# Kernel optimization log

Measured on AMD Instinct MI355X. Metric: run time of the kernel, lower is better.

## Reference

```python
import jax, jax.numpy as jnp
import numpy as np

B, T, DM = 4, 2048, 1024
H, DK, DV = 16, 64, 64


def setup_inputs() -> dict:
    key = jax.random.key(0)
    k1, k2, k3, k4 = jax.random.split(key, 4)
    x = jax.random.normal(k1, (B, T, DM), dtype=jnp.float32)
    scale = 0.02
    Wq = jax.random.normal(k2, (H, DM, DK), dtype=jnp.float32) * scale
    Wk = jax.random.normal(k3, (H, DM, DK), dtype=jnp.float32) * scale
    Wv = jax.random.normal(k4, (H, DM, DV), dtype=jnp.float32) * scale
    return {"x": x, "Wq": Wq, "Wk": Wk, "Wv": Wv}


def reference(x, Wq, Wk, Wv):
    # Per-head projections, vectorized over heads: [B,H,T,dk]
    q = jnp.einsum('btd,hdk->bhtk', x, Wq)
    k = jnp.einsum('btd,hdk->bhtk', x, Wk)
    v = jnp.einsum('btd,hdv->bhtv', x, Wv)
    scale = DK ** -0.5  # k.shape[-1] ** -0.5 in original
    wei = jnp.einsum('bhtk,bhsk->bhts', q, k) * scale  # [B,H,T,T]
    causal = jnp.tril(jnp.ones((T, T), dtype=bool))
    wei = jnp.where(causal, wei, -jnp.inf)
    wei = jax.nn.softmax(wei, axis=-1)
    # dropout p=0.0 -> identity (eval-mode equivalent)
    out = jnp.einsum('bhts,bhsv->bhtv', wei, v)  # [B,H,T,dv]
    # concat heads along last dim: [B,T,H*dv]
    return out.transpose(0, 2, 1, 3).reshape(B, T, H * DV)
```

## Files before the change

### kernel.cpp

```cpp
#include <hip/hip_runtime.h>


#define B_  4
#define T_  2048
#define DM_ 1024
#define H_  16
#define D_  64
#define DMO 1024

typedef unsigned short u16;
typedef unsigned int   u32;
typedef u16   u16x8  __attribute__((ext_vector_type(8)));
typedef short s16x8  __attribute__((ext_vector_type(8)));
typedef float f32x4  __attribute__((ext_vector_type(4)));
typedef float f32x16 __attribute__((ext_vector_type(16)));
typedef u32   u32x2  __attribute__((ext_vector_type(2)));
typedef u32   u32x4  __attribute__((ext_vector_type(4)));

#if __has_builtin(__builtin_amdgcn_exp2f)
#define EXP2(x) __builtin_amdgcn_exp2f(x)
#else
#define EXP2(x) __expf((x) * 0.69314718f)
#endif

#define WAIT_BAR(N) do {                                                      \
    asm volatile("s_waitcnt vmcnt(" #N ")" ::: "memory");                     \
    __builtin_amdgcn_s_barrier();                                             \
    __builtin_amdgcn_sched_barrier(0); } while (0)
#define BAR_ONLY() do {                                                       \
    __builtin_amdgcn_s_barrier();                                             \
    __builtin_amdgcn_sched_barrier(0); } while (0)

__device__ __forceinline__ u16 f2bf_hu(float f) {
    u32 u = __builtin_bit_cast(u32, f) + 0x8000u;
    return (u16)(u >> 16);
}
__device__ __forceinline__ u32 pk2(float lo, float hi) {
    u32 ul = __builtin_bit_cast(u32, lo) + 0x8000u;
    u32 uh = __builtin_bit_cast(u32, hi) + 0x8000u;
    return __builtin_amdgcn_perm(uh, ul, 0x07060302);
}
__device__ __forceinline__ u16x8 cvt8(const float* s) {
    f32x4 a = *(const f32x4*)s;
    f32x4 b = *(const f32x4*)(s + 4);
    u32x4 r { pk2(a[0], a[1]), pk2(a[2], a[3]), pk2(b[0], b[1]), pk2(b[2], b[3]) };
    return __builtin_bit_cast(u16x8, r);
}
__device__ __forceinline__ f32x4 mfma16(u16x8 a, u16x8 b, f32x4 c) {
    return __builtin_amdgcn_mfma_f32_16x16x32_bf16(
        __builtin_bit_cast(s16x8, a), __builtin_bit_cast(s16x8, b), c, 0, 0, 0);
}
__device__ __forceinline__ f32x16 mfma32(u16x8 a, u16x8 b, f32x16 c) {
    return __builtin_amdgcn_mfma_f32_32x32x16_bf16(
        __builtin_bit_cast(s16x8, a), __builtin_bit_cast(s16x8, b), c, 0, 0, 0);
}
__device__ __forceinline__ void gld_lds16(const u16* g, u16* l) {
    __builtin_amdgcn_global_load_lds(
        (const __attribute__((address_space(1))) u32*)g,
        (__attribute__((address_space(3))) u32*)l, 16, 0, 0);
}

__global__ __launch_bounds__(256) void cvt_all(
    const float* __restrict__ x,  const float* __restrict__ Wq,
    const float* __restrict__ Wk, const float* __restrict__ Wv,
    u16* __restrict__ xb, u16* __restrict__ Wt)
{
    __shared__ u16 L[64][74];
    const int bx = blockIdx.x;
    if (bx < 1024) {
        size_t i0 = ((size_t)bx * 256 + threadIdx.x) * 32;
        #pragma unroll
        for (int c = 0; c < 4; c++)
            *(u16x8*)(xb + i0 + c * 8) = cvt8(x + i0 + c * 8);
        return;
    }
    const int wb = bx - 1024;
    const int dblk = wb & 15, h = (wb >> 4) & 15, mat = wb >> 8;
    const float* W = (mat == 0) ? Wq : (mat == 1) ? Wk : Wv;
    const int tid = threadIdx.x;
    {
        const int dl = tid >> 2, c = (tid & 3) * 16;
        const float* src = W + ((size_t)h * DM_ + dblk * 64 + dl) * D_ + c;
        #pragma unroll
        for (int g = 0; g < 2; g++)
            *(u16x8*)&L[dl][c + g * 8] = cvt8(src + g * 8);
    }
    __syncthreads();
    {
        const int dkr = tid >> 2, g = tid & 3;
        u16 tmp[16];
        #pragma unroll
        for (int j = 0; j < 16; j++) tmp[j] = L[g * 16 + j][dkr];
        u16* dst = Wt + ((size_t)(mat * 16 + h) * 64 + dkr) * DM_ + dblk * 64 + g * 16;
        *(u16x8*)dst = *(u16x8*)tmp;
        *(u16x8*)(dst + 8) = *(u16x8*)(tmp + 8);
    }
}

template<int SWAP>
__device__ __forceinline__ void pcompute(const char* Asb, const char* Bsb,
                                         int wm, int wn, int quad, int l16,
                                         int ax, f32x4 (&acc)[4][4]) {
    #pragma unroll
    for (int ks = 0; ks < 2; ks++) {
        u16x8 af[4], bf[4];
        #pragma unroll
        for (int i = 0; i < 4; i++)
            af[i] = *(const u16x8*)(Asb +
                ((((wm * 64 + i * 16 + l16) * 64 + ks * 32 + quad * 8) * 2) ^ ax));
        #pragma unroll
        for (int j = 0; j < 4; j++)
            bf[j] = *(const u16x8*)(Bsb +
                ((((wn * 64 + j * 16 + l16) * 64 + ks * 32 + quad * 8) * 2) ^ ax));
        __builtin_amdgcn_s_setprio(1);
        #pragma unroll
        for (int i = 0; i < 4; i++)
            #pragma unroll
            for (int j = 0; j < 4; j++)
                acc[i][j] = SWAP ? mfma16(bf[j], af[i], acc[i][j])
                                 : mfma16(af[i], bf[j], acc[i][j]);
        __builtin_amdgcn_s_setprio(0);
    }
}

__global__ __launch_bounds__(256) void proj_kernel(
    const u16* __restrict__ xb, const u16* __restrict__ Wt,
    u16* __restrict__ Qc, u16* __restrict__ Kc, u16* __restrict__ Vtc)
{
    __shared__ __attribute__((aligned(16))) u16 As0[128][64];
    __shared__ __attribute__((aligned(16))) u16 Bs0[128][64];
    __shared__ __attribute__((aligned(16))) u16 As1[128][64];
    __shared__ __attribute__((aligned(16))) u16 Bs1[128][64];

    const int pb = blockIdx.x;
    const int wg = (pb & 7) * 192 + (pb >> 3);
    const int m0 = (wg & 63) * 128;
    const int n0 = (wg >> 6) * 128;
    const int mat = n0 >> 10;
    const int tid  = threadIdx.x;
    const int wave = tid >> 6, lane = tid & 63;
    const int quad = lane >> 4, l16 = lane & 15;
    const int wm   = wave >> 1, wn = wave & 1;

    const int r8 = lane >> 3, g8 = lane & 7;
    const int gs = (g8 ^ r8) * 8;
    const int ax = (l16 & 7) << 4;

    f32x4 acc[4][4];
    #pragma unroll
    for (int i = 0; i < 4; i++)
        #pragma unroll
        for (int j = 0; j < 4; j++) acc[i][j] = f32x4{0.f, 0.f, 0.f, 0.f};

    auto STAGE = [&](u16* Ad, u16* Bd, int kb) {
        const int kbase = kb * 64;
        #pragma unroll
        for (int it = 0; it < 4; it++) {
            const int row = it * 32 + wave * 8 + r8;
            const int ldo = (it * 4 + wave) * 512 + lane * 8;
            gld_lds16(xb + (size_t)(m0 + row) * DM_ + kbase + gs, Ad + ldo);
            gld_lds16(Wt + (size_t)(n0 + row) * DM_ + kbase + gs, Bd + ldo);
        }
    };

    STAGE(&As0[0][0], &Bs0[0][0], 0);
    STAGE(&As1[0][0], &Bs1[0][0], 1);

    #define PLOOP(SW)                                                        \
        for (int j = 0; j < 8; j++) {                                        \
            WAIT_BAR(8);                                                     \
            pcompute<SW>((const char*)As0, (const char*)Bs0,                 \
                         wm, wn, quad, l16, ax, acc);                        \
            BAR_ONLY();                                                      \
            if (2 * j + 2 < 16) STAGE(&As0[0][0], &Bs0[0][0], 2 * j + 2);    \
            if (j < 7) { WAIT_BAR(8); } else { WAIT_BAR(0); }                \
            pcompute<SW>((const char*)As1, (const char*)Bs1,                 \
                         wm, wn, quad, l16, ax, acc);                        \
            BAR_ONLY();                                                      \
            if (2 * j + 3 < 16) STAGE(&As1[0][0], &Bs1[0][0], 2 * j + 3);    \
        }
    if (mat != 2) { PLOOP(1) } else { PLOOP(0) }
    #undef PLOOP

    const int h_base = (n0 & 1023) >> 6;
    if (mat != 2) {
        u16* Cm = (mat == 0) ? Qc : Kc;
        const float sc = (mat == 0) ? 0.18033688f : 1.0f;
        #pragma unroll
        for (int i = 0; i < 4; i++) {
            const int m  = m0 + wm * 64 + i * 16 + l16;
            const int bb = m >> 11, t = m & (T_ - 1);
            u16* rowp = Cm + ((size_t)(bb * H_ + h_base + wn) * T_ + t) * D_;
            #pragma unroll
            for (int j = 0; j < 4; j++) {
                const int dk0 = j * 16 + quad * 4;
                u32x2 d { pk2(acc[i][j][0] * sc, acc[i][j][1] * sc),
                          pk2(acc[i][j][2] * sc, acc[i][j][3] * sc) };
                *(u32x2*)(rowp + dk0) = d;
            }
        }
    } else {
        #pragma unroll
        for (int i = 0; i < 4; i++) {
            const int m  = m0 + wm * 64 + i * 16 + quad * 4;
            const int bb = m >> 11, t = m & (T_ - 1);
            #pragma unroll
            for (int j = 0; j < 4; j++) {
                const int dk = j * 16 + l16;
                u32x2 d { pk2(acc[i][j][0], acc[i][j][1]),
                          pk2(acc[i][j][2], acc[i][j][3]) };
                *(u32x2*)(Vtc + ((size_t)(bb * H_ + h_base + wn) * D_ + dk) * T_ + t) = d;
            }
        }
    }
}

__global__ __launch_bounds__(128, 2) void attn_kernel(
    const u16* __restrict__ Qc, const u16* __restrict__ Kc,
    const u16* __restrict__ Vtc, float* __restrict__ out)
{
    __shared__ __attribute__((aligned(16))) u16 Ks0[64][64];
    __shared__ __attribute__((aligned(16))) u16 Vs0[64][64];
    __shared__ __attribute__((aligned(16))) u16 Ks1[64][64];
    __shared__ __attribute__((aligned(16))) u16 Vs1[64][64];

    const int pb = blockIdx.x;
    const int lb = (pb & 7) * 128 + (pb >> 3);
    const int pr = lb & 15;
    const int bh = lb >> 4;
    const int h  = bh & 15, b = bh >> 4;
    const int qa = pr, qb = 31 - pr;

    const int tid = threadIdx.x, w = tid >> 6, lane = tid & 63;
    const int l31 = lane & 31, hi = lane >> 5;
    const int r8 = lane >> 3, g8 = lane & 7;
    const int gs = (g8 ^ r8) * 8;
    const int ax = (l31 & 7) << 4;
    const int qloc = w * 32 + l31;

    const u16* Qbh = Qc + (size_t)(b * H_ + h) * T_ * D_;
    const u16* Kbh = Kc + (size_t)(b * H_ + h) * T_ * D_;
    const u16* Vbh = Vtc + (size_t)(b * H_ + h) * D_ * T_;

    auto TS = [&](int i) { return (i <= qa) ? i : i - qa - 1; };

    auto STAGE = [&](u16* Kd, u16* Vd, int t) {
        const int sbase = t * 64;
        #pragma unroll
        for (int i2 = 0; i2 < 4; i2++) {
            const int seg = i2 * 2 + w;
            const int row = seg * 8 + r8;
            const int ldo = seg * 512 + lane * 8;
            gld_lds16(Kbh + (size_t)(sbase + row) * D_ + gs, Kd + ldo);
            gld_lds16(Vbh + (size_t)row * T_ + sbase + gs,  Vd + ldo);
        }
    };

    int qrow = qa * 64 + qloc;
    u16x8 qf[4];
    #pragma unroll
    for (int ks = 0; ks < 4; ks++)
        qf[ks] = *(const u16x8*)(Qbh + (size_t)qrow * D_ + ks * 16 + hi * 8);

    f32x16 ot0, ot1;
    #pragma unroll
    for (int r = 0; r < 16; r++) { ot0[r] = 0.f; ot1[r] = 0.f; }
    float mi = -1e30f, li = 0.f;

    auto EPI = [&]() {
        const float inv = 1.0f / li;
        float* orow = out + (size_t)(b * T_ + qrow) * DMO + h * D_;
        #pragma unroll
        for (int c = 0; c < 2; c++)
            #pragma unroll
            for (int hf = 0; hf < 2; hf++) {
                f32x4 v0, v1;
                #pragma unroll
                for (int j = 0; j < 4; j++) {
                    v0[j] = ot0[c * 8 + hf * 4 + j] * inv;
                    v1[j] = ot1[c * 8 + hf * 4 + j] * inv;
                }
                *(f32x4*)(orow + c * 16 + hf * 8 + hi * 4)      = v0;
                *(f32x4*)(orow + 32 + c * 16 + hf * 8 + hi * 4) = v1;
            }
    };

    auto COMPUTE = [&](const char* Ksb, const char* Vsb, int i) {
        f32x16 st0, st1;
        #pragma unroll
        for (int r = 0; r < 16; r++) { st0[r] = 0.f; st1[r] = 0.f; }
        __builtin_amdgcn_s_setprio(1);
        #pragma unroll
        for (int ks = 0; ks < 4; ks++) {
            const int co = (ks * 16 + hi * 8) * 2;
            u16x8 k0 = *(const u16x8*)(Ksb + ((l31 * 128 + co) ^ ax));
            u16x8 k1 = *(const u16x8*)(Ksb + (((32 + l31) * 128 + co) ^ ax));
            st0 = mfma32(k0, qf[ks], st0);
            st1 = mfma32(k1, qf[ks], st1);
        }
        __builtin_amdgcn_s_setprio(0);

        if (i == qa || i == 32) {
            #pragma unroll
            for (int r = 0; r < 16; r++) {
                const int sl = (r & 3) + 8 * (r >> 2) + 4 * hi;
                if (sl > qloc)      st0[r] = -1e30f;
                if (sl + 32 > qloc) st1[r] = -1e30f;
            }
        }

        float mx = -1e30f;
        #pragma unroll
        for (int r = 0; r < 16; r++) mx = fmaxf(mx, fmaxf(st0[r], st1[r]));
        mx = fmaxf(mx, __shfl_xor(mx, 32));
        if (!__all(mx - mi <= 8.f)) {
            const float mn = fmaxf(mi, mx);
            const float al = EXP2(mi - mn);
            li *= al;
            #pragma unroll
            for (int r = 0; r < 16; r++) { ot0[r] *= al; ot1[r] *= al; }
            mi = mn;
        }
        float sum = 0.f;
        #pragma unroll
        for (int r = 0; r < 16; r++) {
            const float p0 = EXP2(st0[r] - mi);
            const float p1 = EXP2(st1[r] - mi);
            st0[r] = p0; st1[r] = p1;
            sum += p0 + p1;
        }
        sum += __shfl_xor(sum, 32);
        li += sum;

        u16x8 pb4[4];
        #define PACK(SRC, C, OUT) {                                           \
            u32 d0 = pk2(SRC[8*(C)+0], SRC[8*(C)+1]);                         \
            u32 d1 = pk2(SRC[8*(C)+2], SRC[8*(C)+3]);                         \
            u32 d2 = pk2(SRC[8*(C)+4], SRC[8*(C)+5]);                         \
            u32 d3 = pk2(SRC[8*(C)+6], SRC[8*(C)+7]);                         \
            u32 e0 = __shfl_xor(hi ? d0 : d2, 32);                            \
            u32 e1 = __shfl_xor(hi ? d1 : d3, 32);                            \
            u32x4 wds{ hi ? e0 : d0, hi ? e1 : d1,                            \
                       hi ? d2 : e0, hi ? d3 : e1 };                          \
            OUT = __builtin_bit_cast(u16x8, wds); }
        PACK(st0, 0, pb4[0]); PACK(st0, 1, pb4[1]);
        PACK(st1, 0, pb4[2]); PACK(st1, 1, pb4[3]);
        #undef PACK

        __builtin_amdgcn_s_setprio(1);
        #pragma unroll
        for (int kc = 0; kc < 4; kc++) {
            const int co = (kc * 16 + hi * 8) * 2;
            u16x8 v0 = *(const u16x8*)(Vsb + ((l31 * 128 + co) ^ ax));
            u16x8 v1 = *(const u16x8*)(Vsb + (((32 + l31) * 128 + co) ^ ax));
            ot0 = mfma32(v0, pb4[kc], ot0);
            ot1 = mfma32(v1, pb4[kc], ot1);
        }
        __builtin_amdgcn_s_setprio(0);

        if (i == qa) {
            EPI();
            qrow = qb * 64 + qloc;
            #pragma unroll
            for (int ks = 0; ks < 4; ks++)
                qf[ks] = *(const u16x8*)(Qbh + (size_t)qrow * D_ + ks * 16 + hi * 8);
            #pragma unroll
            for (int r = 0; r < 16; r++) { ot0[r] = 0.f; ot1[r] = 0.f; }
            mi = -1e30f; li = 0.f;
        }
    };

    STAGE(&Ks0[0][0], &Vs0[0][0], 0);
    STAGE(&Ks1[0][0], &Vs1[0][0], TS(1));

    for (int j = 0; j < 16; j++) {
        const int i0 = 2 * j, i1 = 2 * j + 1;
        WAIT_BAR(8);
        COMPUTE((const char*)Ks0, (const char*)Vs0, i0);
        BAR_ONLY();
        if (i0 + 2 <= 32) STAGE(&Ks0[0][0], &Vs0[0][0], TS(i0 + 2));
        WAIT_BAR(8);
        COMPUTE((const char*)Ks1, (const char*)Vs1, i1);
        BAR_ONLY();
        if (i1 + 2 <= 32) STAGE(&Ks1[0][0], &Vs1[0][0], TS(i1 + 2));
    }
    WAIT_BAR(0);
    COMPUTE((const char*)Ks0, (const char*)Vs0, 32);
    EPI();
}

extern "C" void kernel_launch(void* const* d_in, const int* in_sizes, int n_in,
                              void* d_out, int out_size, void* d_ws, size_t ws_size,
                              hipStream_t stream) {
    int xi = 0, wi[3] = {1, 2, 3};
    {
        int k = 0, found = 0;
        for (int i = 0; i < n_in && i < 8; i++) {
            if (in_sizes[i] == B_ * T_ * DM_) { xi = i; found = 1; }
            else if (in_sizes[i] == H_ * DM_ * D_ && k < 3) wi[k++] = i;
        }
        if (!found || k != 3) { xi = 0; wi[0] = 1; wi[1] = 2; wi[2] = 3; }
    }
    const float* x  = (const float*)d_in[xi];
    const float* Wq = (const float*)d_in[wi[0]];
    const float* Wk = (const float*)d_in[wi[1]];
    const float* Wv = (const float*)d_in[wi[2]];
    float* out = (float*)d_out;

    u16* xb = (u16*)d_out;
    u16* Wt = xb + (size_t)B_ * T_ * DM_;
    const size_t per = (size_t)B_ * H_ * T_ * D_;
    u16* Qc  = (u16*)d_ws;
    u16* Kc  = Qc + per;
    u16* Vtc = Kc + per;

    cvt_all<<<1792, 256, 0, stream>>>(x, Wq, Wk, Wv, xb, Wt);
    proj_kernel<<<1536, 256, 0, stream>>>(xb, Wt, Qc, Kc, Vtc);
    attn_kernel<<<1024, 128, 0, stream>>>(Qc, Kc, Vtc, out);
}
```

Baseline: 233.0 us.

## Restructure causal attention into 8-wave blocks sharing K/V tiles over 256 query rows

Replaces the 2-wave blocks, which processed a paired (qa, 31-qa) query tile sequence for causal load balance, with 512-thread blocks covering 256 contiguous query rows. All eight waves share each staged K/V tile, and each wave skips compute past its own diagonal tile. This raises K/V reuse per LDS load and cuts global traffic, but gives up the paired balancing. Per-block work now varies with the row group; heavy groups are launched first and waves idle at barriers once past their diagonal.

```diff
diff --git a/kernel.cpp b/kernel.cpp
--- a/kernel.cpp
+++ b/kernel.cpp
@@ -215,7 +215,7 @@
     }
 }
 
-__global__ __launch_bounds__(128, 2) void attn_kernel(
+__global__ __launch_bounds__(512, 2) void attn_kernel(
     const u16* __restrict__ Qc, const u16* __restrict__ Kc,
     const u16* __restrict__ Vtc, float* __restrict__ out)
 {
@@ -224,39 +224,34 @@
     __shared__ __attribute__((aligned(16))) u16 Ks1[64][64];
     __shared__ __attribute__((aligned(16))) u16 Vs1[64][64];
 
-    const int pb = blockIdx.x;
-    const int lb = (pb & 7) * 128 + (pb >> 3);
-    const int pr = lb & 15;
-    const int bh = lb >> 4;
-    const int h  = bh & 15, b = bh >> 4;
-    const int qa = pr, qb = 31 - pr;
+    const int pb  = blockIdx.x;
+    const int bh  = (pb & 7) * 8 + ((pb >> 3) & 7);
+    const int g   = 7 - (pb >> 6);
+    const int h   = bh & 15, b = bh >> 4;
 
     const int tid = threadIdx.x, w = tid >> 6, lane = tid & 63;
     const int l31 = lane & 31, hi = lane >> 5;
-    const int r8 = lane >> 3, g8 = lane & 7;
+    const int r8 = (tid >> 3) & 7, g8 = tid & 7;
     const int gs = (g8 ^ r8) * 8;
     const int ax = (l31 & 7) << 4;
-    const int qloc = w * 32 + l31;
+
+    const int qrow = g * 256 + w * 32 + l31;
+    const int i_d  = g * 4 + (w >> 1);
+    const int nt   = g * 4 + 4;
+    const int qmask = 32 * (w & 1) + l31;
 
     const u16* Qbh = Qc + (size_t)(b * H_ + h) * T_ * D_;
     const u16* Kbh = Kc + (size_t)(b * H_ + h) * T_ * D_;
     const u16* Vbh = Vtc + (size_t)(b * H_ + h) * D_ * T_;
 
-    auto TS = [&](int i) { return (i <= qa) ? i : i - qa - 1; };
-
     auto STAGE = [&](u16* Kd, u16* Vd, int t) {
         const int sbase = t * 64;
-        #pragma unroll
-        for (int i2 = 0; i2 < 4; i2++) {
-            const int seg = i2 * 2 + w;
-            const int row = seg * 8 + r8;
-            const int ldo = seg * 512 + lane * 8;
-            gld_lds16(Kbh + (size_t)(sbase + row) * D_ + gs, Kd + ldo);
-            gld_lds16(Vbh + (size_t)row * T_ + sbase + gs,  Vd + ldo);
-        }
+        const int row = tid >> 3;
+        const int ldo = tid * 8;
+        gld_lds16(Kbh + (size_t)(sbase + row) * D_ + gs, Kd + ldo);
+        gld_lds16(Vbh + (size_t)row * T_ + sbase + gs,  Vd + ldo);
     };
 
-    int qrow = qa * 64 + qloc;
     u16x8 qf[4];
     #pragma unroll
     for (int ks = 0; ks < 4; ks++)
@@ -266,24 +261,6 @@
     #pragma unroll
     for (int r = 0; r < 16; r++) { ot0[r] = 0.f; ot1[r] = 0.f; }
     float mi = -1e30f, li = 0.f;
-
-    auto EPI = [&]() {
-        const float inv = 1.0f / li;
-        float* orow = out + (size_t)(b * T_ + qrow) * DMO + h * D_;
-        #pragma unroll
-        for (int c = 0; c < 2; c++)
-            #pragma unroll
-            for (int hf = 0; hf < 2; hf++) {
-                f32x4 v0, v1;
-                #pragma unroll
-                for (int j = 0; j < 4; j++) {
-                    v0[j] = ot0[c * 8 + hf * 4 + j] * inv;
-                    v1[j] = ot1[c * 8 + hf * 4 + j] * inv;
-                }
-                *(f32x4*)(orow + c * 16 + hf * 8 + hi * 4)      = v0;
-                *(f32x4*)(orow + 32 + c * 16 + hf * 8 + hi * 4) = v1;
-            }
-    };
 
     auto COMPUTE = [&](const char* Ksb, const char* Vsb, int i) {
         f32x16 st0, st1;
@@ -300,12 +277,12 @@
         }
         __builtin_amdgcn_s_setprio(0);
 
-        if (i == qa || i == 32) {
+        if (i == i_d) {
             #pragma unroll
             for (int r = 0; r < 16; r++) {
                 const int sl = (r & 3) + 8 * (r >> 2) + 4 * hi;
-                if (sl > qloc)      st0[r] = -1e30f;
-                if (sl + 32 > qloc) st1[r] = -1e30f;
+                if (sl > qmask)      st0[r] = -1e30f;
+                if (sl + 32 > qmask) st1[r] = -1e30f;
             }
         }
 
@@ -357,36 +334,39 @@
             ot1 = mfma32(v1, pb4[kc], ot1);
         }
         __builtin_amdgcn_s_setprio(0);
-
-        if (i == qa) {
-            EPI();
-            qrow = qb * 64 + qloc;
-            #pragma unroll
-            for (int ks = 0; ks < 4; ks++)
-                qf[ks] = *(const u16x8*)(Qbh + (size_t)qrow * D_ + ks * 16 + hi * 8);
-            #pragma unroll
-            for (int r = 0; r < 16; r++) { ot0[r] = 0.f; ot1[r] = 0.f; }
-            mi = -1e30f; li = 0.f;
-        }
     };
 
     STAGE(&Ks0[0][0], &Vs0[0][0], 0);
-    STAGE(&Ks1[0][0], &Vs1[0][0], TS(1));
-
-    for (int j = 0; j < 16; j++) {
+    STAGE(&Ks1[0][0], &Vs1[0][0], 1);
+
+    const int np = nt >> 1;
+    for (int j = 0; j < np; j++) {
         const int i0 = 2 * j, i1 = 2 * j + 1;
-        WAIT_BAR(8);
-        COMPUTE((const char*)Ks0, (const char*)Vs0, i0);
+        WAIT_BAR(2);
+        if (i0 <= i_d) COMPUTE((const char*)Ks0, (const char*)Vs0, i0);
         BAR_ONLY();
-        if (i0 + 2 <= 32) STAGE(&Ks0[0][0], &Vs0[0][0], TS(i0 + 2));
-        WAIT_BAR(8);
-        COMPUTE((const char*)Ks1, (const char*)Vs1, i1);
+        if (i0 + 2 < nt) STAGE(&Ks0[0][0], &Vs0[0][0], i0 + 2);
+        if (j < np - 1) { WAIT_BAR(2); } else { WAIT_BAR(0); }
+        if (i1 <= i_d) COMPUTE((const char*)Ks1, (const char*)Vs1, i1);
         BAR_ONLY();
-        if (i1 + 2 <= 32) STAGE(&Ks1[0][0], &Vs1[0][0], TS(i1 + 2));
-    }
-    WAIT_BAR(0);
-    COMPUTE((const char*)Ks0, (const char*)Vs0, 32);
-    EPI();
+        if (i1 + 2 < nt) STAGE(&Ks1[0][0], &Vs1[0][0], i1 + 2);
+    }
+
+    const float inv = 1.0f / li;
+    float* orow = out + (size_t)(b * T_ + qrow) * DMO + h * D_;
+    #pragma unroll
+    for (int c = 0; c < 2; c++)
+        #pragma unroll
+        for (int hf = 0; hf < 2; hf++) {
+            f32x4 v0, v1;
+            #pragma unroll
+            for (int j = 0; j < 4; j++) {
+                v0[j] = ot0[c * 8 + hf * 4 + j] * inv;
+                v1[j] = ot1[c * 8 + hf * 4 + j] * inv;
+            }
+            *(f32x4*)(orow + c * 16 + hf * 8 + hi * 4)      = v0;
+            *(f32x4*)(orow + 32 + c * 16 + hf * 8 + hi * 4) = v1;
+        }
 }
 
 extern "C" void kernel_launch(void* const* d_in, const int* in_sizes, int n_in,
@@ -416,5 +396,5 @@
 
     cvt_all<<<1792, 256, 0, stream>>>(x, Wq, Wk, Wv, xb, Wt);
     proj_kernel<<<1536, 256, 0, stream>>>(xb, Wt, Qc, Kc, Vtc);
-    attn_kernel<<<1024, 128, 0, stream>>>(Qc, Kc, Vtc, out);
-}
+    attn_kernel<<<512, 512, 0, stream>>>(Qc, Kc, Vtc, out);
+}
```

Result: faster. 227.0 us (-2.6%).
